# Performance work log

Measured on AMD Instinct MI355X. Metric: run time of the kernel, lower is better.

The kernel has to match this reference:

```python
import jax, jax.numpy as jnp
import numpy as np

N_EXPERTS = 16
TOP_K = 2
D_MODEL = 1024
D_FF = 1024
D_FF_SHARED = 2048
T_TOKENS = 4096


def setup_inputs() -> dict:
    key = jax.random.key(0)
    ks = jax.random.split(key, 7)
    s = 0.02
    return {
        "hidden_states": jax.random.normal(ks[0], (T_TOKENS, D_MODEL), jnp.float32),
        "gate_weight": jax.random.normal(ks[1], (N_EXPERTS, D_MODEL), jnp.float32) * s,
        "expert_gate_up": jax.random.normal(ks[2], (N_EXPERTS, 2 * D_FF, D_MODEL), jnp.float32) * s,
        "expert_down": jax.random.normal(ks[3], (N_EXPERTS, D_MODEL, D_FF), jnp.float32) * s,
        "shared_gate_up": jax.random.normal(ks[4], (2 * D_FF_SHARED, D_MODEL), jnp.float32) * s,
        "shared_down": jax.random.normal(ks[5], (D_MODEL, D_FF_SHARED), jnp.float32) * s,
        "shared_expert_gate_weight": jax.random.normal(ks[6], (1, D_MODEL), jnp.float32) * s,
    }


def _moe_forward(x, gate_weight, expert_gate_up, expert_down):
    T = x.shape[0]
    E = gate_weight.shape[0]
    # Router: top-k over logits, softmax over the selected logits (fp32)
    router_logits = x @ gate_weight.T                      # [T, E]
    topk_logits, topk_ids = jax.lax.top_k(router_logits, TOP_K)
    topk_weights = jax.nn.softmax(topk_logits.astype(jnp.float32), axis=-1)
    # Dense combine matrix C[t, e] = routing weight of expert e for token t
    combine = jnp.zeros((T, E), jnp.float32).at[
        jnp.arange(T)[:, None], topk_ids
    ].add(topk_weights)                                    # [T, E]

    # Scan over experts to avoid materializing [E, T, d]
    def body(acc, inputs):
        w_gu, w_d, c_e = inputs                            # [2F,d], [d,F], [T]
        gu = x @ w_gu.T                                    # [T, 2F]
        g, u = gu[:, :D_FF], gu[:, D_FF:]
        h = jax.nn.silu(g) * u                             # [T, F]
        acc = acc + c_e[:, None] * (h @ w_d.T)             # [T, d]
        return acc, None

    acc0 = jnp.zeros_like(x)
    moe_out, _ = jax.lax.scan(body, acc0, (expert_gate_up, expert_down, combine.T))
    return moe_out


def _shared_expert(x, shared_gate_up, shared_down, shared_expert_gate_weight):
    gu = x @ shared_gate_up.T                              # [T, 2Fs]
    mid = gu.shape[-1] // 2
    h = jax.nn.silu(gu[:, :mid]) * gu[:, mid:]
    out = h @ shared_down.T                                # [T, d]
    gate = jax.nn.sigmoid(x @ shared_expert_gate_weight.T)  # [T, 1]
    return out * gate


def reference(hidden_states, gate_weight, expert_gate_up, expert_down,
              shared_gate_up, shared_down, shared_expert_gate_weight):
    moe_out = _moe_forward(hidden_states, gate_weight, expert_gate_up, expert_down)
    shared_out = _shared_expert(hidden_states, shared_gate_up, shared_down,
                                shared_expert_gate_weight)
    return moe_out + shared_out
```

## Files before the change

kernel.cpp:

```cpp
#include <hip/hip_runtime.h>
#include <hip/hip_bf16.h>

#define T_TOKENS 4096
#define D_MODEL  1024
#define N_EXP    16
#define D_FF     1024
#define D_FF_SH  2048
#define MAX_T256 48

typedef __attribute__((ext_vector_type(8))) short short8;
typedef __attribute__((ext_vector_type(4))) float float4v;

__device__ __forceinline__ short f2bf(float f) {
    union { float f; unsigned u; } c; c.f = f;
    unsigned u = c.u + 0x7fffu + ((c.u >> 16) & 1u);
    return (short)(u >> 16);
}

__device__ __forceinline__ void gload16(const void* g, void* l) {
    __builtin_amdgcn_global_load_lds(
        (const __attribute__((address_space(1))) void*)g,
        (__attribute__((address_space(3))) void*)l, 16, 0, 0);
}

__global__ __launch_bounds__(256) void convert_all_kernel(
    const float* __restrict__ s0, short* __restrict__ d0,
    const float* __restrict__ s1, short* __restrict__ d1,
    const float* __restrict__ s2, short* __restrict__ d2,
    const float* __restrict__ s3, short* __restrict__ d3) {
    int c = blockIdx.x * 256 + threadIdx.x;
    const float* s; short* d; int off;
    if      (c < 4194304) { s = s0; d = d0; off = c; }
    else if (c < 6291456) { s = s1; d = d1; off = c - 4194304; }
    else if (c < 6815744) { s = s2; d = d2; off = c - 6291456; }
    else                  { s = s3; d = d3; off = c - 6815744; }
    size_t i = (size_t)off * 8;
    float4 a = *(const float4*)(s + i);
    float4 b = *(const float4*)(s + i + 4);
    union { short sh[8]; int4 v; } p;
    p.sh[0] = f2bf(a.x); p.sh[1] = f2bf(a.y); p.sh[2] = f2bf(a.z); p.sh[3] = f2bf(a.w);
    p.sh[4] = f2bf(b.x); p.sh[5] = f2bf(b.y); p.sh[6] = f2bf(b.z); p.sh[7] = f2bf(b.w);
    *(int4*)(d + i) = p.v;
}

__global__ __launch_bounds__(256) void router_kernel(
    const float* __restrict__ x, const float* __restrict__ gw, const float* __restrict__ sgw,
    short* __restrict__ xb, int* __restrict__ topk_id, float* __restrict__ topk_w,
    float* __restrict__ gate, int* __restrict__ counts) {
    __shared__ float gwl[17 * 1024];
    int tid = threadIdx.x;
#pragma unroll
    for (int i = 0; i < 16; i++)
        *(float4*)&gwl[tid * 4 + i * 1024] = *(const float4*)&gw[tid * 4 + i * 1024];
    *(float4*)&gwl[16384 + tid * 4] = *(const float4*)&sgw[tid * 4];
    __syncthreads();

    int wave = tid >> 6, lane = tid & 63;
    int t0 = blockIdx.x * 16 + wave * 4;

    float acc[4][17];
#pragma unroll
    for (int tt = 0; tt < 4; tt++)
#pragma unroll
        for (int e = 0; e < 17; e++) acc[tt][e] = 0.f;

#pragma unroll
    for (int i = 0; i < 4; i++) {
        int d = lane * 4 + i * 256;
        float4 xv[4];
#pragma unroll
        for (int tt = 0; tt < 4; tt++) {
            xv[tt] = *(const float4*)&x[(size_t)(t0 + tt) * D_MODEL + d];
            union { short sh[4]; int2 v; } p;
            p.sh[0] = f2bf(xv[tt].x); p.sh[1] = f2bf(xv[tt].y);
            p.sh[2] = f2bf(xv[tt].z); p.sh[3] = f2bf(xv[tt].w);
            *(int2*)&xb[(size_t)(t0 + tt) * D_MODEL + d] = p.v;
        }
#pragma unroll
        for (int e = 0; e < 17; e++) {
            float4 g = *(const float4*)&gwl[e * 1024 + d];
#pragma unroll
            for (int tt = 0; tt < 4; tt++)
                acc[tt][e] += xv[tt].x * g.x + xv[tt].y * g.y + xv[tt].z * g.z + xv[tt].w * g.w;
        }
    }

#pragma unroll
    for (int tt = 0; tt < 4; tt++)
#pragma unroll
        for (int e = 0; e < 17; e++)
            for (int off = 32; off; off >>= 1) acc[tt][e] += __shfl_xor(acc[tt][e], off);

    if (lane == 0) {
#pragma unroll
        for (int tt = 0; tt < 4; tt++) {
            int t = t0 + tt;
            float v1 = -1e30f, v2 = -1e30f; int i1 = 0, i2 = 0;
#pragma unroll
            for (int e = 0; e < 16; e++) {
                float v = acc[tt][e];
                if (v > v1) { v2 = v1; i2 = i1; v1 = v; i1 = e; }
                else if (v > v2) { v2 = v; i2 = e; }
            }
            float e2 = expf(v2 - v1);
            float s = 1.f + e2;
            topk_id[t * 2] = i1; topk_id[t * 2 + 1] = i2;
            topk_w[t * 2] = 1.f / s; topk_w[t * 2 + 1] = e2 / s;
            gate[t] = 1.f / (1.f + expf(-acc[tt][16]));
            atomicAdd(&counts[i1], 1); atomicAdd(&counts[i2], 1);
        }
    }
}

__global__ void offsets_kernel(const int* __restrict__ counts, int* __restrict__ offsets,
                               int* __restrict__ cursor, int* __restrict__ tile_map,
                               int* __restrict__ n_tiles) {
    if (threadIdx.x == 0) {
        int off = 0, nt = 0;
        for (int e = 0; e < N_EXP; e++) {
            offsets[e] = off; cursor[e] = off;
            int c = counts[e];
            for (int r = 0; r < c; r += 256) tile_map[nt++] = (e << 16) | (r >> 8);
            off += c;
        }
        n_tiles[0] = nt;
    }
}

__global__ __launch_bounds__(256) void scatter_kernel(
    const int* __restrict__ topk_id, const float* __restrict__ topk_w,
    int* __restrict__ cursor, int* __restrict__ tok_list, float* __restrict__ tok_w,
    int* __restrict__ slot_of) {
    int t = blockIdx.x * 256 + threadIdx.x;
#pragma unroll
    for (int k = 0; k < 2; k++) {
        int e = topk_id[t * 2 + k];
        int pos = atomicAdd(&cursor[e], 1);
        tok_list[pos] = t;
        tok_w[pos] = topk_w[t * 2 + k];
        slot_of[t * 2 + k] = pos;
    }
}

__global__ __launch_bounds__(512, 2) void gemm1_kernel(
    const short* __restrict__ xb,
    const short* __restrict__ Wexp,
    const short* __restrict__ Wsh,
    short* __restrict__ Hexp,
    short* __restrict__ Hsh,
    const int* __restrict__ tok_list,
    const int* __restrict__ offsets, const int* __restrict__ counts,
    const int* __restrict__ tile_map, const int* __restrict__ n_tiles) {
    int bx = blockIdx.x, by = blockIdx.y;
    int count, row0, dff;
    const int* idx = nullptr;
    const short* Wg; short* Hout;
    if (bx < MAX_T256) {
        if (by >= 8 || bx >= n_tiles[0]) return;
        int tm = tile_map[bx];
        int e = tm >> 16; row0 = (tm & 0xffff) << 8;
        count = counts[e];
        int base = offsets[e];
        idx = tok_list + base;
        Wg = Wexp + (size_t)e * 2 * D_FF * D_MODEL;
        Hout = Hexp + (size_t)base * D_FF;
        dff = D_FF;
    } else {
        row0 = (bx - MAX_T256) * 256; count = T_TOKENS;
        Wg = Wsh; Hout = Hsh; dff = D_FF_SH;
    }
    int col0 = by * 128;
    const short* Wu = Wg + (size_t)dff * D_MODEL;

    __shared__ char lds[65536];

    int t = threadIdx.x;
    int wave = t >> 6, lane = t & 63;
    int wm = (wave & 3) * 64, wn = (wave >> 2) * 64;
    int fr = lane & 15, fk2 = (lane >> 4) * 16;

    float4v accg[4][4], accu[4][4];
#pragma unroll
    for (int i = 0; i < 4; i++)
#pragma unroll
        for (int j = 0; j < 4; j++) { accg[i][j] = (float4v)0.f; accu[i][j] = (float4v)0.f; }

    int rA = t >> 2;
    int cq = (t & 3) * 8;
    int r0c = min(row0 + rA, count - 1);
    int r1c = min(row0 + rA + 128, count - 1);
    int g0 = idx ? idx[r0c] : r0c;
    int g1 = idx ? idx[r1c] : r1c;
    const short* aP0 = xb + (size_t)g0 * D_MODEL + cq;
    const short* aP1 = xb + (size_t)g1 * D_MODEL + cq;
    const short* bgP = Wg + (size_t)(col0 + rA) * D_MODEL + cq;
    const short* buP = Wu + (size_t)(col0 + rA) * D_MODEL + cq;
    int lo = t * 16;

    gload16(aP0, lds + lo);
    gload16(aP1, lds + 8192 + lo);
    gload16(bgP, lds + 16384 + lo);
    gload16(buP, lds + 24576 + lo);

    const int NK = D_MODEL / 32;
    for (int k = 0; k < NK; k++) {
        __syncthreads();
        if (k + 1 < NK) {
            int s = ((k + 1) & 1) * 32768;
            int off = (k + 1) * 32;
            gload16(aP0 + off, lds + s + lo);
            gload16(aP1 + off, lds + s + 8192 + lo);
            gload16(bgP + off, lds + s + 16384 + lo);
            gload16(buP + off, lds + s + 24576 + lo);
        }
        int sb = (k & 1) * 32768;
        short8 af[4], bgf[4], buf[4];
#pragma unroll
        for (int i = 0; i < 4; i++)
            af[i] = *(const short8*)(lds + sb + (wm + i * 16 + fr) * 64 + fk2);
#pragma unroll
        for (int j = 0; j < 4; j++) {
            bgf[j] = *(const short8*)(lds + sb + 16384 + (wn + j * 16 + fr) * 64 + fk2);
            buf[j] = *(const short8*)(lds + sb + 24576 + (wn + j * 16 + fr) * 64 + fk2);
        }
#pragma unroll
        for (int i = 0; i < 4; i++)
#pragma unroll
            for (int j = 0; j < 4; j++) {
                accg[i][j] = __builtin_amdgcn_mfma_f32_16x16x32_bf16(af[i], bgf[j], accg[i][j], 0, 0, 0);
                accu[i][j] = __builtin_amdgcn_mfma_f32_16x16x32_bf16(af[i], buf[j], accu[i][j], 0, 0, 0);
            }
    }

    int erow = (lane >> 4) * 4;
    int ecol = lane & 15;
#pragma unroll
    for (int i = 0; i < 4; i++)
#pragma unroll
        for (int j = 0; j < 4; j++)
#pragma unroll
            for (int r = 0; r < 4; r++) {
                int row = wm + i * 16 + erow + r;
                if (row0 + row < count) {
                    float g = accg[i][j][r], u = accu[i][j][r];
                    float h = g / (1.f + expf(-g)) * u;
                    Hout[(size_t)(row0 + row) * dff + col0 + wn + j * 16 + ecol] = f2bf(h);
                }
            }
}

__global__ __launch_bounds__(512, 2) void gemm2_kernel(
    const short* __restrict__ Hexp, const short* __restrict__ Hsh,
    const short* __restrict__ Wdexp,
    const short* __restrict__ Wdsh,
    float* __restrict__ oslots,
    float* __restrict__ out,
    const float* __restrict__ tok_w, const float* __restrict__ gate,
    const int* __restrict__ offsets, const int* __restrict__ counts,
    const int* __restrict__ tile_map, const int* __restrict__ n_tiles) {
    int bx = blockIdx.x, by = blockIdx.y;
    int count, row0, K, base;
    const short* Ab; const short* B;
    bool shared_part;
    if (bx < MAX_T256) {
        if (bx >= n_tiles[0]) return;
        int tm = tile_map[bx];
        int e = tm >> 16; row0 = (tm & 0xffff) << 8;
        count = counts[e]; base = offsets[e];
        Ab = Hexp + (size_t)base * D_FF; K = D_FF;
        B = Wdexp + (size_t)e * D_MODEL * D_FF;
        shared_part = false;
    } else {
        row0 = (bx - MAX_T256) * 256; count = T_TOKENS; base = 0;
        Ab = Hsh; K = D_FF_SH; B = Wdsh; shared_part = true;
    }
    int col0 = by * 128;

    __shared__ char lds[49152];

    int t = threadIdx.x;
    int wave = t >> 6, lane = t & 63;
    int wm = (wave & 3) * 64, wn = (wave >> 2) * 64;
    int fr = lane & 15, fk2 = (lane >> 4) * 16;

    float4v acc[4][4];
#pragma unroll
    for (int i = 0; i < 4; i++)
#pragma unroll
        for (int j = 0; j < 4; j++) acc[i][j] = (float4v)0.f;

    int rA = t >> 2;
    int cq = (t & 3) * 8;
    int r0c = min(row0 + rA, count - 1);
    int r1c = min(row0 + rA + 128, count - 1);
    const short* aP0 = Ab + (size_t)r0c * K + cq;
    const short* aP1 = Ab + (size_t)r1c * K + cq;
    const short* bP  = B + (size_t)(col0 + rA) * K + cq;
    int lo = t * 16;

    gload16(aP0, lds + lo);
    gload16(aP1, lds + 8192 + lo);
    gload16(bP,  lds + 16384 + lo);

    const int NK = K / 32;
    for (int k = 0; k < NK; k++) {
        __syncthreads();
        if (k + 1 < NK) {
            int s = ((k + 1) & 1) * 24576;
            int off = (k + 1) * 32;
            gload16(aP0 + off, lds + s + lo);
            gload16(aP1 + off, lds + s + 8192 + lo);
            gload16(bP + off,  lds + s + 16384 + lo);
        }
        int sb = (k & 1) * 24576;
        short8 af[4], bf[4];
#pragma unroll
        for (int i = 0; i < 4; i++)
            af[i] = *(const short8*)(lds + sb + (wm + i * 16 + fr) * 64 + fk2);
#pragma unroll
        for (int j = 0; j < 4; j++)
            bf[j] = *(const short8*)(lds + sb + 16384 + (wn + j * 16 + fr) * 64 + fk2);
#pragma unroll
        for (int i = 0; i < 4; i++)
#pragma unroll
            for (int j = 0; j < 4; j++)
                acc[i][j] = __builtin_amdgcn_mfma_f32_16x16x32_bf16(af[i], bf[j], acc[i][j], 0, 0, 0);
    }

    int erow = (lane >> 4) * 4;
    int ecol = lane & 15;
#pragma unroll
    for (int i = 0; i < 4; i++)
#pragma unroll
        for (int j = 0; j < 4; j++)
#pragma unroll
            for (int r = 0; r < 4; r++) {
                int row = wm + i * 16 + erow + r;
                if (row0 + row < count) {
                    float v = acc[i][j][r];
                    int col = col0 + wn + j * 16 + ecol;
                    if (!shared_part) {
                        int slot = base + row0 + row;
                        oslots[(size_t)slot * D_MODEL + col] = tok_w[slot] * v;
                    } else {
                        out[(size_t)(row0 + row) * D_MODEL + col] = gate[row0 + row] * v;
                    }
                }
            }
}

__global__ __launch_bounds__(256) void combine_kernel(
    float* __restrict__ out, const float* __restrict__ oslots,
    const int* __restrict__ slot_of) {
    int t = blockIdx.x;
    int sA = slot_of[t * 2], sB = slot_of[t * 2 + 1];
    int d = threadIdx.x * 4;
    float4 o = *(float4*)&out[(size_t)t * D_MODEL + d];
    float4 a = *(const float4*)&oslots[(size_t)sA * D_MODEL + d];
    float4 b = *(const float4*)&oslots[(size_t)sB * D_MODEL + d];
    o.x += a.x + b.x; o.y += a.y + b.y; o.z += a.z + b.z; o.w += a.w + b.w;
    *(float4*)&out[(size_t)t * D_MODEL + d] = o;
}

extern "C" void kernel_launch(void* const* d_in, const int* in_sizes, int n_in,
                              void* d_out, int out_size, void* d_ws, size_t ws_size,
                              hipStream_t stream) {
    const float* x     = (const float*)d_in[0];
    const float* gw    = (const float*)d_in[1];
    const float* egu   = (const float*)d_in[2];
    const float* edown = (const float*)d_in[3];
    const float* sgu   = (const float*)d_in[4];
    const float* sdown = (const float*)d_in[5];
    const float* sgate = (const float*)d_in[6];
    float* out = (float*)d_out;
    char* ws = (char*)d_ws;

    const size_t XB_OFF     = 0;
    const size_t WGU_OFF    = XB_OFF     + (size_t)4096*1024*2;
    const size_t WDOWN_OFF  = WGU_OFF    + (size_t)16*2048*1024*2;
    const size_t WSGU_OFF   = WDOWN_OFF  + (size_t)16*1024*1024*2;
    const size_t WSDOWN_OFF = WSGU_OFF   + (size_t)4096*1024*2;
    const size_t HEXP_OFF   = WSDOWN_OFF + (size_t)1024*2048*2;
    const size_t HSH_OFF    = HEXP_OFF   + (size_t)8192*1024*2;
    const size_t OSLOT_OFF  = HSH_OFF    + (size_t)4096*2048*2;
    const size_t TID_OFF    = OSLOT_OFF  + (size_t)8192*1024*4;
    const size_t TW_OFF     = TID_OFF    + 4096*2*4;
    const size_t GATE_OFF   = TW_OFF     + 4096*2*4;
    const size_t TOKL_OFF   = GATE_OFF   + 4096*4;
    const size_t TOKW_OFF   = TOKL_OFF   + 8192*4;
    const size_t SLOT_OFF   = TOKW_OFF   + 8192*4;
    const size_t CNT_OFF    = SLOT_OFF   + 8192*4;
    const size_t OFFS_OFF   = CNT_OFF    + 256;
    const size_t CUR_OFF    = OFFS_OFF   + 256;
    const size_t TMAP_OFF   = CUR_OFF    + 256;
    const size_t NT_OFF     = TMAP_OFF   + 512;

    short* xb      = (short*)(ws + XB_OFF);
    short* wgu_b   = (short*)(ws + WGU_OFF);
    short* wdown_b = (short*)(ws + WDOWN_OFF);
    short* wsgu_b  = (short*)(ws + WSGU_OFF);
    short* wsdn_b  = (short*)(ws + WSDOWN_OFF);
    short* h_exp   = (short*)(ws + HEXP_OFF);
    short* h_sh    = (short*)(ws + HSH_OFF);
    float* oslots  = (float*)(ws + OSLOT_OFF);
    int*   topk_id = (int*)(ws + TID_OFF);
    float* topk_w  = (float*)(ws + TW_OFF);
    float* gate    = (float*)(ws + GATE_OFF);
    int*   tok_l   = (int*)(ws + TOKL_OFF);
    float* tok_w   = (float*)(ws + TOKW_OFF);
    int*   slot_of = (int*)(ws + SLOT_OFF);
    int*   counts  = (int*)(ws + CNT_OFF);
    int*   offsets = (int*)(ws + OFFS_OFF);
    int*   cursor  = (int*)(ws + CUR_OFF);
    int*   tmap    = (int*)(ws + TMAP_OFF);
    int*   ntiles  = (int*)(ws + NT_OFF);

    hipMemsetAsync(counts, 0, 64, stream);

    convert_all_kernel<<<27648, 256, 0, stream>>>(egu, wgu_b, edown, wdown_b,
                                                  sgu, wsgu_b, sdown, wsdn_b);
    router_kernel<<<256, 256, 0, stream>>>(x, gw, sgate, xb, topk_id, topk_w, gate, counts);
    offsets_kernel<<<1, 64, 0, stream>>>(counts, offsets, cursor, tmap, ntiles);
    scatter_kernel<<<T_TOKENS / 256, 256, 0, stream>>>(topk_id, topk_w, cursor, tok_l, tok_w, slot_of);

    gemm1_kernel<<<dim3(MAX_T256 + 16, 16), 512, 0, stream>>>(
        xb, wgu_b, wsgu_b, h_exp, h_sh, tok_l, offsets, counts, tmap, ntiles);

    gemm2_kernel<<<dim3(MAX_T256 + 16, 8), 512, 0, stream>>>(
        h_exp, h_sh, wdown_b, wsdn_b, oslots, out, tok_w, gate, offsets, counts, tmap, ntiles);

    combine_kernel<<<T_TOKENS, 256, 0, stream>>>(out, oslots, slot_of);
}
```

Measured before the change: 602.9 us.

## Deepen LDS ring-buffer pipelining and swizzle LDS layout in both GEMM kernels

Replaces double-buffered LDS staging with a 4-stage ring in the gate/up kernel and a 6-stage ring in the down kernel. Each iteration waits with explicit vmcnt counts instead of a full drain before the barrier. It also XOR-style rotates the 16-byte chunk placement on both the write and read side to cut LDS bank conflicts, and raises wave priority around the MFMA block. The larger LDS footprint (128-144 KB) limits occupancy to one block per CU, and it relies on correct hand-set waitcnt values.

```diff
diff --git a/kernel.cpp b/kernel.cpp
--- a/kernel.cpp
+++ b/kernel.cpp
@@ -22,6 +22,11 @@
         (const __attribute__((address_space(1))) void*)g,
         (__attribute__((address_space(3))) void*)l, 16, 0, 0);
 }
+
+#define RING_TOP(VM) do { \
+    asm volatile("s_waitcnt vmcnt(" #VM ") lgkmcnt(0)" ::: "memory"); \
+    __builtin_amdgcn_s_barrier(); \
+} while (0)
 
 __global__ __launch_bounds__(256) void convert_all_kernel(
     const float* __restrict__ s0, short* __restrict__ d0,
@@ -172,12 +177,13 @@
     int col0 = by * 128;
     const short* Wu = Wg + (size_t)dff * D_MODEL;
 
-    __shared__ char lds[65536];
+    __shared__ char lds[131072];
 
     int t = threadIdx.x;
     int wave = t >> 6, lane = t & 63;
     int wm = (wave & 3) * 64, wn = (wave >> 2) * 64;
-    int fr = lane & 15, fk2 = (lane >> 4) * 16;
+    int fr = lane & 15;
+    int fk2p = ((((lane >> 4) + (fr >> 1)) & 3) << 4);
 
     float4v accg[4][4], accu[4][4];
 #pragma unroll
@@ -186,7 +192,8 @@
         for (int j = 0; j < 4; j++) { accg[i][j] = (float4v)0.f; accu[i][j] = (float4v)0.f; }
 
     int rA = t >> 2;
-    int cq = (t & 3) * 8;
+    int csrc = ((t & 3) - (t >> 3)) & 3;
+    int cq = csrc * 8;
     int r0c = min(row0 + rA, count - 1);
     int r1c = min(row0 + rA + 128, count - 1);
     int g0 = idx ? idx[r0c] : r0c;
@@ -197,40 +204,47 @@
     const short* buP = Wu + (size_t)(col0 + rA) * D_MODEL + cq;
     int lo = t * 16;
 
-    gload16(aP0, lds + lo);
-    gload16(aP1, lds + 8192 + lo);
-    gload16(bgP, lds + 16384 + lo);
-    gload16(buP, lds + 24576 + lo);
-
-    const int NK = D_MODEL / 32;
-    for (int k = 0; k < NK; k++) {
-        __syncthreads();
-        if (k + 1 < NK) {
-            int s = ((k + 1) & 1) * 32768;
-            int off = (k + 1) * 32;
-            gload16(aP0 + off, lds + s + lo);
-            gload16(aP1 + off, lds + s + 8192 + lo);
-            gload16(bgP + off, lds + s + 16384 + lo);
-            gload16(buP + off, lds + s + 24576 + lo);
+    auto stage = [&](int s) {
+        char* base = lds + (s & 3) * 32768;
+        int off = s * 32;
+        gload16(aP0 + off, base + lo);
+        gload16(aP1 + off, base + 8192 + lo);
+        gload16(bgP + off, base + 16384 + lo);
+        gload16(buP + off, base + 24576 + lo);
+    };
+    auto compute = [&](int k) {
+        const char* sb = lds + (k & 3) * 32768;
+        short8 af[4], bgf[4], buf4[4];
+#pragma unroll
+        for (int i = 0; i < 4; i++)
+            af[i] = *(const short8*)(sb + (wm + i * 16 + fr) * 64 + fk2p);
+#pragma unroll
+        for (int j = 0; j < 4; j++) {
+            bgf[j] = *(const short8*)(sb + 16384 + (wn + j * 16 + fr) * 64 + fk2p);
+            buf4[j] = *(const short8*)(sb + 24576 + (wn + j * 16 + fr) * 64 + fk2p);
         }
-        int sb = (k & 1) * 32768;
-        short8 af[4], bgf[4], buf[4];
-#pragma unroll
-        for (int i = 0; i < 4; i++)
-            af[i] = *(const short8*)(lds + sb + (wm + i * 16 + fr) * 64 + fk2);
-#pragma unroll
-        for (int j = 0; j < 4; j++) {
-            bgf[j] = *(const short8*)(lds + sb + 16384 + (wn + j * 16 + fr) * 64 + fk2);
-            buf[j] = *(const short8*)(lds + sb + 24576 + (wn + j * 16 + fr) * 64 + fk2);
-        }
+        __builtin_amdgcn_s_setprio(1);
 #pragma unroll
         for (int i = 0; i < 4; i++)
 #pragma unroll
             for (int j = 0; j < 4; j++) {
                 accg[i][j] = __builtin_amdgcn_mfma_f32_16x16x32_bf16(af[i], bgf[j], accg[i][j], 0, 0, 0);
-                accu[i][j] = __builtin_amdgcn_mfma_f32_16x16x32_bf16(af[i], buf[j], accu[i][j], 0, 0, 0);
+                accu[i][j] = __builtin_amdgcn_mfma_f32_16x16x32_bf16(af[i], buf4[j], accu[i][j], 0, 0, 0);
             }
-    }
+        __builtin_amdgcn_s_setprio(0);
+    };
+
+    const int NK = D_MODEL / 32;
+    stage(0); stage(1); stage(2);
+    int k = 0;
+    for (; k < NK - 3; ++k) {
+        RING_TOP(8);
+        stage(k + 3);
+        compute(k);
+    }
+    RING_TOP(8); compute(k); ++k;
+    RING_TOP(4); compute(k); ++k;
+    RING_TOP(0); compute(k);
 
     int erow = (lane >> 4) * 4;
     int ecol = lane & 15;
@@ -276,12 +290,13 @@
     }
     int col0 = by * 128;
 
-    __shared__ char lds[49152];
+    __shared__ char lds[147456];
 
     int t = threadIdx.x;
     int wave = t >> 6, lane = t & 63;
     int wm = (wave & 3) * 64, wn = (wave >> 2) * 64;
-    int fr = lane & 15, fk2 = (lane >> 4) * 16;
+    int fr = lane & 15;
+    int fk2p = ((((lane >> 4) + (fr >> 1)) & 3) << 4);
 
     float4v acc[4][4];
 #pragma unroll
@@ -290,7 +305,8 @@
         for (int j = 0; j < 4; j++) acc[i][j] = (float4v)0.f;
 
     int rA = t >> 2;
-    int cq = (t & 3) * 8;
+    int csrc = ((t & 3) - (t >> 3)) & 3;
+    int cq = csrc * 8;
     int r0c = min(row0 + rA, count - 1);
     int r1c = min(row0 + rA + 128, count - 1);
     const short* aP0 = Ab + (size_t)r0c * K + cq;
@@ -298,34 +314,44 @@
     const short* bP  = B + (size_t)(col0 + rA) * K + cq;
     int lo = t * 16;
 
-    gload16(aP0, lds + lo);
-    gload16(aP1, lds + 8192 + lo);
-    gload16(bP,  lds + 16384 + lo);
-
-    const int NK = K / 32;
-    for (int k = 0; k < NK; k++) {
-        __syncthreads();
-        if (k + 1 < NK) {
-            int s = ((k + 1) & 1) * 24576;
-            int off = (k + 1) * 32;
-            gload16(aP0 + off, lds + s + lo);
-            gload16(aP1 + off, lds + s + 8192 + lo);
-            gload16(bP + off,  lds + s + 16384 + lo);
-        }
-        int sb = (k & 1) * 24576;
+    auto stage = [&](int pos, int s) {
+        char* bb = lds + pos * 24576;
+        int off = s * 32;
+        gload16(aP0 + off, bb + lo);
+        gload16(aP1 + off, bb + 8192 + lo);
+        gload16(bP + off,  bb + 16384 + lo);
+    };
+    auto compute = [&](int pos) {
+        const char* sb = lds + pos * 24576;
         short8 af[4], bf[4];
 #pragma unroll
         for (int i = 0; i < 4; i++)
-            af[i] = *(const short8*)(lds + sb + (wm + i * 16 + fr) * 64 + fk2);
+            af[i] = *(const short8*)(sb + (wm + i * 16 + fr) * 64 + fk2p);
 #pragma unroll
         for (int j = 0; j < 4; j++)
-            bf[j] = *(const short8*)(lds + sb + 16384 + (wn + j * 16 + fr) * 64 + fk2);
+            bf[j] = *(const short8*)(sb + 16384 + (wn + j * 16 + fr) * 64 + fk2p);
+        __builtin_amdgcn_s_setprio(1);
 #pragma unroll
         for (int i = 0; i < 4; i++)
 #pragma unroll
             for (int j = 0; j < 4; j++)
                 acc[i][j] = __builtin_amdgcn_mfma_f32_16x16x32_bf16(af[i], bf[j], acc[i][j], 0, 0, 0);
-    }
+        __builtin_amdgcn_s_setprio(0);
+    };
+
+    const int NK = K / 32;
+    stage(0, 0); stage(1, 1); stage(2, 2); stage(3, 3); stage(4, 4);
+    int k = 0, spos = 5, cpos = 0;
+    for (; k < NK - 5; ++k) {
+        RING_TOP(12);
+        stage(spos, k + 5); spos = (spos == 5) ? 0 : spos + 1;
+        compute(cpos);      cpos = (cpos == 5) ? 0 : cpos + 1;
+    }
+    RING_TOP(12); compute(cpos); cpos = (cpos == 5) ? 0 : cpos + 1; ++k;
+    RING_TOP(9);  compute(cpos); cpos = (cpos == 5) ? 0 : cpos + 1; ++k;
+    RING_TOP(6);  compute(cpos); cpos = (cpos == 5) ? 0 : cpos + 1; ++k;
+    RING_TOP(3);  compute(cpos); cpos = (cpos == 5) ? 0 : cpos + 1; ++k;
+    RING_TOP(0);  compute(cpos);
 
     int erow = (lane >> 4) * 4;
     int ecol = lane & 15;
```

Result: no change. 606.5 us (+0.6%).
